# Kernel tuning notes

Hardware: AMD Instinct MI355X
Metric: run time of the kernel (lower is better)

The kernel has to match this reference:

```python
import jax, jax.numpy as jnp
import numpy as np

B, N, CQ, CH, H = 4, 1024, 512, 512, 8
D = CH // H  # head_dim = 64


def setup_inputs() -> dict:
    key = jax.random.key(0)
    ks = jax.random.split(key, 8)
    s = jnp.float32(0.02)  # realistic (non-degenerate) init scale instead of the module's zeros
    return {
        "q_x": jax.random.normal(ks[0], (B, N, CQ), jnp.float32),
        "attn_bias": jax.random.normal(ks[1], (B, H, N, N), jnp.float32),
        "Wq": jax.random.normal(ks[2], (CH, CQ), jnp.float32) * s,
        "bq": jnp.zeros((CH,), jnp.float32),
        "Wk": jax.random.normal(ks[3], (CH, CQ), jnp.float32) * s,  # LinearNoBias
        "Wv": jax.random.normal(ks[4], (CH, CQ), jnp.float32) * s,  # LinearNoBias
        "Wo": jax.random.normal(ks[5], (CQ, CH), jnp.float32) * s,
        "bo": jnp.zeros((CQ,), jnp.float32),
        "Wg": jax.random.normal(ks[6], (CQ, CQ), jnp.float32) * s,
        "bg": jnp.zeros((CQ,), jnp.float32),
        "gating_bias": jnp.ones((CQ,), jnp.float32),
    }


def reference(q_x, attn_bias, Wq, bq, Wk, Wv, Wo, bo, Wg, bg, gating_bias):
    Bq, Nq, _ = q_x.shape
    scale = jnp.asarray(D, q_x.dtype) ** -0.5
    # QKV projections; self-attention path (q_x is kv_x, ndim==3) applies scale to q
    q = (q_x @ Wq.T + bq).reshape(Bq, Nq, H, D).transpose(0, 2, 1, 3) * scale  # [B,H,N,D]
    k = (q_x @ Wk.T).reshape(Bq, Nq, H, D).transpose(0, 2, 1, 3)               # [B,H,N,D]
    v = (q_x @ Wv.T).reshape(Bq, Nq, H, D).transpose(0, 2, 1, 3)               # [B,H,N,D]
    # bias-augmented attention
    logits = jnp.einsum("bhqd,bhkd->bhqk", q, k) + attn_bias                    # [B,H,N,N]
    a = jax.nn.softmax(logits, axis=-1)
    o = jnp.einsum("bhqk,bhkd->bhqd", a, v)                                     # [B,H,N,D]
    o = o.transpose(0, 2, 1, 3).reshape(Bq, Nq, CH)                             # flatten heads
    out = o @ Wo.T + bo                                                         # to_out: c_hidden -> c_q
    # sigmoid gating with learned gating_bias (init ones)
    gate = jax.nn.sigmoid(q_x @ Wg.T + bg + gating_bias)
    return out * gate
```

## Files before the change

### kernel.cpp

```cpp
#include <hip/hip_runtime.h>
#include <math.h>


typedef __bf16 bf16x8 __attribute__((ext_vector_type(8)));
typedef float f32x4 __attribute__((ext_vector_type(4)));

__device__ __forceinline__ unsigned short f2bf(float f) {
    union { float f; unsigned u; } v; v.f = f;
    unsigned r = v.u + 0x7fff + ((v.u >> 16) & 1);
    return (unsigned short)(r >> 16);
}

__device__ __forceinline__ bf16x8 ldb8(const unsigned short* p) {
    union { float4 f; bf16x8 b; } u;
    u.f = *(const float4*)p;
    return u.b;
}

__device__ __forceinline__ void ld16(unsigned short* l, const unsigned short* g) {
    __builtin_amdgcn_global_load_lds(
        (const __attribute__((address_space(1))) unsigned*)g,
        (__attribute__((address_space(3))) unsigned*)l, 16, 0, 0);
}

__global__ __launch_bounds__(256) void convert_kernel(
    const float* __restrict__ X, const float* __restrict__ Wq,
    const float* __restrict__ Wk, const float* __restrict__ Wg,
    const float* __restrict__ Wv, const float* __restrict__ Wo,
    unsigned short* __restrict__ Xb, unsigned short* __restrict__ Wcat)
{
    int i4 = (blockIdx.x * 256 + threadIdx.x) * 4;
    const float* src;
    unsigned short* dst;
    int off;
    if (i4 < 2097152) {
        src = X; dst = Xb; off = i4;
    } else {
        int g = i4 - 2097152;
        int sect = g >> 18;
        src = (sect == 0) ? Wq : (sect == 1) ? Wk : (sect == 2) ? Wg
            : (sect == 3) ? Wv : Wo;
        dst = Wcat + (sect << 18);
        off = g & 262143;
    }
    float4 v = *(const float4*)&src[off];
    ushort4 u;
    u.x = f2bf(v.x); u.y = f2bf(v.y); u.z = f2bf(v.z); u.w = f2bf(v.w);
    *(ushort4*)&dst[off] = u;
}

__device__ __forceinline__ void gemm_core(
    const unsigned short* __restrict__ Ag,
    const unsigned short* __restrict__ Bg,
    unsigned short* __restrict__ Ab, unsigned short* __restrict__ Bb,
    f32x4 acc[4][4])
{
    const int tid = threadIdx.x;
    const int lane = tid & 63;
    const int quad = lane >> 4, lx = lane & 15;
    const int wid = tid >> 6;
    const int mw0 = (wid >> 1) * 64, nw0 = (wid & 1) * 64;
    const int r0 = tid >> 2, c0 = (tid & 3) * 8;
    const int r1 = (tid + 256) >> 2, c1 = (tid & 3) * 8;
    unsigned short* lA0 = Ab + ((tid & ~63) << 3);
    unsigned short* lA1 = Ab + (((tid & ~63) + 256) << 3);
    unsigned short* lB0 = Bb + ((tid & ~63) << 3);
    unsigned short* lB1 = Bb + (((tid & ~63) + 256) << 3);

    for (int k0 = 0; k0 < 512; k0 += 32) {
        ld16(lA0, &Ag[(size_t)r0 * 512 + k0 + c0]);
        ld16(lA1, &Ag[(size_t)r1 * 512 + k0 + c1]);
        ld16(lB0, &Bg[(size_t)r0 * 512 + k0 + c0]);
        ld16(lB1, &Bg[(size_t)r1 * 512 + k0 + c1]);
        __syncthreads();
        bf16x8 af[4], bfr[4];
#pragma unroll
        for (int mi = 0; mi < 4; ++mi)
            af[mi] = ldb8(&Ab[(mw0 + mi * 16 + lx) * 32 + quad * 8]);
#pragma unroll
        for (int ni = 0; ni < 4; ++ni)
            bfr[ni] = ldb8(&Bb[(nw0 + ni * 16 + lx) * 32 + quad * 8]);
#pragma unroll
        for (int mi = 0; mi < 4; ++mi)
#pragma unroll
            for (int ni = 0; ni < 4; ++ni)
                acc[mi][ni] = __builtin_amdgcn_mfma_f32_16x16x32_bf16(
                    af[mi], bfr[ni], acc[mi][ni], 0, 0, 0);
        __syncthreads();
    }
}

__global__ __launch_bounds__(256) void proj_gemm(
    const unsigned short* __restrict__ Xb, const unsigned short* __restrict__ Wcat,
    const float* __restrict__ bq, const float* __restrict__ bg,
    const float* __restrict__ gbias,
    unsigned short* __restrict__ qb, unsigned short* __restrict__ kb,
    unsigned short* __restrict__ vtb, float* __restrict__ gateb)
{
    __shared__ __align__(16) unsigned short Ab[128 * 32];
    __shared__ __align__(16) unsigned short Bb[128 * 32];
    const int row0 = blockIdx.x * 128;
    const int colv0 = blockIdx.y * 128;
    f32x4 acc[4][4];
#pragma unroll
    for (int i = 0; i < 4; ++i)
#pragma unroll
        for (int j = 0; j < 4; ++j) acc[i][j] = (f32x4){0.f, 0.f, 0.f, 0.f};

    gemm_core(Xb + (size_t)row0 * 512, Wcat + (size_t)colv0 * 512, Ab, Bb, acc);

    const int tid = threadIdx.x;
    const int lane = tid & 63;
    const int quad = lane >> 4, lx = lane & 15;
    const int wid = tid >> 6;
    const int mw0 = (wid >> 1) * 64, nw0 = (wid & 1) * 64;
    const int wsel = colv0 >> 9;
    const int ncb = colv0 & 511;

    if (wsel == 0) {
#pragma unroll
        for (int mi = 0; mi < 4; ++mi) {
#pragma unroll
            for (int ni = 0; ni < 4; ++ni) {
                int ch = ncb + nw0 + ni * 16 + lx;
                int h = ch >> 6, d = ch & 63;
                float bias = bq[ch];
#pragma unroll
                for (int r = 0; r < 4; ++r) {
                    int m = row0 + mw0 + mi * 16 + quad * 4 + r;
                    int b = m >> 10, nn = m & 1023;
                    qb[(size_t)(b * 8 + h) * 65536 + (size_t)nn * 64 + d] =
                        f2bf((acc[mi][ni][r] + bias) * 0.125f);
                }
            }
        }
    } else if (wsel == 1) {
#pragma unroll
        for (int mi = 0; mi < 4; ++mi) {
#pragma unroll
            for (int ni = 0; ni < 4; ++ni) {
                int ch = ncb + nw0 + ni * 16 + lx;
                int h = ch >> 6, d = ch & 63;
#pragma unroll
                for (int r = 0; r < 4; ++r) {
                    int m = row0 + mw0 + mi * 16 + quad * 4 + r;
                    int b = m >> 10, nn = m & 1023;
                    kb[(size_t)(b * 8 + h) * 65536 + (size_t)nn * 64 + d] =
                        f2bf(acc[mi][ni][r]);
                }
            }
        }
    } else if (wsel == 2) {
#pragma unroll
        for (int mi = 0; mi < 4; ++mi) {
#pragma unroll
            for (int ni = 0; ni < 4; ++ni) {
                int ch = ncb + nw0 + ni * 16 + lx;
                float bias = bg[ch] + gbias[ch];
#pragma unroll
                for (int r = 0; r < 4; ++r) {
                    int m = row0 + mw0 + mi * 16 + quad * 4 + r;
                    float z = acc[mi][ni][r] + bias;
                    gateb[(size_t)m * 512 + ch] = 1.f / (1.f + __expf(-z));
                }
            }
        }
    } else {
#pragma unroll
        for (int mi = 0; mi < 4; ++mi) {
            int tok0 = row0 + mw0 + mi * 16 + quad * 4;
            int b = tok0 >> 10, nn0 = tok0 & 1023;
#pragma unroll
            for (int ni = 0; ni < 4; ++ni) {
                int ch = ncb + nw0 + ni * 16 + lx;
                int h = ch >> 6, d = ch & 63;
                ushort4 u;
                u.x = f2bf(acc[mi][ni][0]);
                u.y = f2bf(acc[mi][ni][1]);
                u.z = f2bf(acc[mi][ni][2]);
                u.w = f2bf(acc[mi][ni][3]);
                *(ushort4*)&vtb[(size_t)(b * 8 + h) * 65536 + (size_t)d * 1024 + nn0] = u;
            }
        }
    }
}

#define LSTR 72

__global__ __launch_bounds__(256) void attn_kernel(
    const unsigned short* __restrict__ qb, const unsigned short* __restrict__ kb,
    const unsigned short* __restrict__ vtb, const float* __restrict__ bias,
    unsigned short* __restrict__ obb)
{
    __shared__ unsigned short Qs[64 * LSTR];
    __shared__ unsigned short Ks[64 * LSTR];
    __shared__ unsigned short Vt[64 * LSTR];
    __shared__ unsigned short Ps[64 * LSTR];

    const int tid = threadIdx.x;
    const int bh = blockIdx.y;
    const int qr0 = blockIdx.x * 64;
    const int wv = tid >> 6, lane = tid & 63;
    const int quad = lane >> 4, lx = lane & 15;
    const int qw0 = wv * 16;

    const unsigned short* qp = qb + (size_t)bh * 65536;
    const unsigned short* kp = kb + (size_t)bh * 65536;
    const unsigned short* vp = vtb + (size_t)bh * 65536;
    const float* bp = bias + (size_t)bh * 1048576;

    const int sr0 = tid >> 3, sc0 = (tid & 7) * 8;
    const int sr1 = (tid + 256) >> 3, sc1 = (tid & 7) * 8;

    *(float4*)&Qs[sr0 * LSTR + sc0] = *(const float4*)&qp[(size_t)(qr0 + sr0) * 64 + sc0];
    *(float4*)&Qs[sr1 * LSTR + sc1] = *(const float4*)&qp[(size_t)(qr0 + sr1) * 64 + sc1];

    float4 kr0 = *(const float4*)&kp[(size_t)sr0 * 64 + sc0];
    float4 kr1 = *(const float4*)&kp[(size_t)sr1 * 64 + sc1];
    float4 vr0 = *(const float4*)&vp[(size_t)sr0 * 1024 + sc0];
    float4 vr1 = *(const float4*)&vp[(size_t)sr1 * 1024 + sc1];

    const float* bbase = bp + (size_t)(qr0 + qw0 + quad * 4) * 1024 + lx;
    float bv[4][4];
#pragma unroll
    for (int r = 0; r < 4; ++r)
#pragma unroll
        for (int c = 0; c < 4; ++c)
            bv[r][c] = bbase[(size_t)r * 1024 + c * 16];

    __syncthreads();

    bf16x8 aq0 = ldb8(&Qs[(qw0 + lx) * LSTR + quad * 8]);
    bf16x8 aq1 = ldb8(&Qs[(qw0 + lx) * LSTR + 32 + quad * 8]);

    float l_i[4] = {0.f, 0.f, 0.f, 0.f};
    f32x4 oacc[4];
#pragma unroll
    for (int c = 0; c < 4; ++c) oacc[c] = (f32x4){0.f, 0.f, 0.f, 0.f};

#pragma unroll 1
    for (int kt = 0; kt < 16; ++kt) {
        __syncthreads();
        *(float4*)&Ks[sr0 * LSTR + sc0] = kr0;
        *(float4*)&Ks[sr1 * LSTR + sc1] = kr1;
        *(float4*)&Vt[sr0 * LSTR + sc0] = vr0;
        *(float4*)&Vt[sr1 * LSTR + sc1] = vr1;
        __syncthreads();

        const int ktn = (kt + 1) & 15;
        kr0 = *(const float4*)&kp[(size_t)(ktn * 64 + sr0) * 64 + sc0];
        kr1 = *(const float4*)&kp[(size_t)(ktn * 64 + sr1) * 64 + sc1];
        vr0 = *(const float4*)&vp[(size_t)sr0 * 1024 + ktn * 64 + sc0];
        vr1 = *(const float4*)&vp[(size_t)sr1 * 1024 + ktn * 64 + sc1];
        float bvn[4][4];
#pragma unroll
        for (int r = 0; r < 4; ++r)
#pragma unroll
            for (int c = 0; c < 4; ++c)
                bvn[r][c] = bbase[(size_t)r * 1024 + ktn * 64 + c * 16];

        f32x4 sacc[4];
#pragma unroll
        for (int c = 0; c < 4; ++c) {
            bf16x8 bk0 = ldb8(&Ks[(c * 16 + lx) * LSTR + quad * 8]);
            bf16x8 bk1 = ldb8(&Ks[(c * 16 + lx) * LSTR + 32 + quad * 8]);
            f32x4 z = {0.f, 0.f, 0.f, 0.f};
            z = __builtin_amdgcn_mfma_f32_16x16x32_bf16(aq0, bk0, z, 0, 0, 0);
            z = __builtin_amdgcn_mfma_f32_16x16x32_bf16(aq1, bk1, z, 0, 0, 0);
            sacc[c] = z;
        }

#pragma unroll
        for (int r = 0; r < 4; ++r) {
            float p0 = __expf(sacc[0][r] + bv[r][0]);
            float p1 = __expf(sacc[1][r] + bv[r][1]);
            float p2 = __expf(sacc[2][r] + bv[r][2]);
            float p3 = __expf(sacc[3][r] + bv[r][3]);
            l_i[r] += p0 + p1 + p2 + p3;
            int prow = (qw0 + quad * 4 + r) * LSTR;
            Ps[prow + 0 * 16 + lx] = f2bf(p0);
            Ps[prow + 1 * 16 + lx] = f2bf(p1);
            Ps[prow + 2 * 16 + lx] = f2bf(p2);
            Ps[prow + 3 * 16 + lx] = f2bf(p3);
        }

        bf16x8 ap0 = ldb8(&Ps[(qw0 + lx) * LSTR + quad * 8]);
        bf16x8 ap1 = ldb8(&Ps[(qw0 + lx) * LSTR + 32 + quad * 8]);
#pragma unroll
        for (int c = 0; c < 4; ++c) {
            bf16x8 bv0 = ldb8(&Vt[(c * 16 + lx) * LSTR + quad * 8]);
            bf16x8 bv1 = ldb8(&Vt[(c * 16 + lx) * LSTR + 32 + quad * 8]);
            oacc[c] = __builtin_amdgcn_mfma_f32_16x16x32_bf16(ap0, bv0, oacc[c], 0, 0, 0);
            oacc[c] = __builtin_amdgcn_mfma_f32_16x16x32_bf16(ap1, bv1, oacc[c], 0, 0, 0);
        }

#pragma unroll
        for (int r = 0; r < 4; ++r)
#pragma unroll
            for (int c = 0; c < 4; ++c)
                bv[r][c] = bvn[r][c];
    }

    const int b = bh >> 3, h = bh & 7;
#pragma unroll
    for (int r = 0; r < 4; ++r) {
        float lt = l_i[r];
        lt += __shfl_xor(lt, 1);
        lt += __shfl_xor(lt, 2);
        lt += __shfl_xor(lt, 4);
        lt += __shfl_xor(lt, 8);
        float inv = 1.f / lt;
        int row = qr0 + qw0 + quad * 4 + r;
        unsigned short* op = obb + (size_t)(b * 1024 + row) * 512 + h * 64 + lx;
#pragma unroll
        for (int c = 0; c < 4; ++c)
            op[c * 16] = f2bf(oacc[c][r] * inv);
    }
}

__global__ __launch_bounds__(256) void out_gemm(
    const unsigned short* __restrict__ obb, const unsigned short* __restrict__ WoB,
    const float* __restrict__ bo, const float* __restrict__ gateb,
    float* __restrict__ out)
{
    __shared__ __align__(16) unsigned short Ab[128 * 32];
    __shared__ __align__(16) unsigned short Bb[128 * 32];
    const int row0 = blockIdx.x * 128;
    const int n0 = blockIdx.y * 128;
    f32x4 acc[4][4];
#pragma unroll
    for (int i = 0; i < 4; ++i)
#pragma unroll
        for (int j = 0; j < 4; ++j) acc[i][j] = (f32x4){0.f, 0.f, 0.f, 0.f};

    gemm_core(obb + (size_t)row0 * 512, WoB + (size_t)n0 * 512, Ab, Bb, acc);

    const int tid = threadIdx.x;
    const int lane = tid & 63;
    const int quad = lane >> 4, lx = lane & 15;
    const int wid = tid >> 6;
    const int mw0 = (wid >> 1) * 64, nw0 = (wid & 1) * 64;

#pragma unroll
    for (int mi = 0; mi < 4; ++mi) {
#pragma unroll
        for (int ni = 0; ni < 4; ++ni) {
            int n = n0 + nw0 + ni * 16 + lx;
            float bias = bo[n];
#pragma unroll
            for (int r = 0; r < 4; ++r) {
                int m = row0 + mw0 + mi * 16 + quad * 4 + r;
                out[(size_t)m * 512 + n] =
                    (acc[mi][ni][r] + bias) * gateb[(size_t)m * 512 + n];
            }
        }
    }
}

extern "C" void kernel_launch(void* const* d_in, const int* in_sizes, int n_in,
                              void* d_out, int out_size, void* d_ws, size_t ws_size,
                              hipStream_t stream) {
    (void)in_sizes; (void)n_in; (void)out_size; (void)ws_size;
    const float* q_x   = (const float*)d_in[0];
    const float* bias  = (const float*)d_in[1];
    const float* Wq    = (const float*)d_in[2];
    const float* bq    = (const float*)d_in[3];
    const float* Wk    = (const float*)d_in[4];
    const float* Wv    = (const float*)d_in[5];
    const float* Wo    = (const float*)d_in[6];
    const float* bo    = (const float*)d_in[7];
    const float* Wg    = (const float*)d_in[8];
    const float* bg    = (const float*)d_in[9];
    const float* gbias = (const float*)d_in[10];
    float* out = (float*)d_out;

    char* ws = (char*)d_ws;
    unsigned short* qb   = (unsigned short*)ws;
    unsigned short* kb   = (unsigned short*)(ws + (4u << 20));
    unsigned short* vtb  = (unsigned short*)(ws + (8u << 20));
    float* gateb         = (float*)(ws + (12u << 20));
    unsigned short* obb  = (unsigned short*)(ws + (20u << 20));
    unsigned short* Xb   = (unsigned short*)(ws + (24u << 20));
    unsigned short* Wcat = (unsigned short*)(ws + (28u << 20));

    convert_kernel<<<3328, 256, 0, stream>>>(q_x, Wq, Wk, Wg, Wv, Wo, Xb, Wcat);
    proj_gemm<<<dim3(32, 16), dim3(256), 0, stream>>>(
        Xb, Wcat, bq, bg, gbias, qb, kb, vtb, gateb);
    attn_kernel<<<dim3(16, 32), dim3(256), 0, stream>>>(qb, kb, vtb, bias, obb);
    out_gemm<<<dim3(32, 4), dim3(256), 0, stream>>>(
        obb, Wcat + (size_t)2048 * 512, bo, gateb, out);
}
```

Measured before the change: 268.4 us.

## Register-prefetch GEMM tiles into padded LDS, shrink out_gemm tile, merge attn buffers

The GEMM core stops using direct global-to-LDS loads. It now prefetches the next K-slice into registers while the MFMAs run on the current one, and stores tiles with a padded stride to cut bank conflicts. out_gemm switches to 64-row tiles, doubling its grid so more CUs get work. The attention kernel reuses the Q buffer for P to cut shared memory, which could raise occupancy. The register prefetch adds register pressure and costs VGPR-to-LDS store instructions.

```diff
diff --git a/kernel.cpp b/kernel.cpp
--- a/kernel.cpp
+++ b/kernel.cpp
@@ -15,12 +15,6 @@
     union { float4 f; bf16x8 b; } u;
     u.f = *(const float4*)p;
     return u.b;
-}
-
-__device__ __forceinline__ void ld16(unsigned short* l, const unsigned short* g) {
-    __builtin_amdgcn_global_load_lds(
-        (const __attribute__((address_space(1))) unsigned*)g,
-        (__attribute__((address_space(3))) unsigned*)l, 16, 0, 0);
 }
 
 __global__ __launch_bounds__(256) void convert_kernel(
@@ -49,6 +43,8 @@
     *(ushort4*)&dst[off] = u;
 }
 
+#define GSTR 40
+
 __device__ __forceinline__ void gemm_core(
     const unsigned short* __restrict__ Ag,
     const unsigned short* __restrict__ Bg,
@@ -60,26 +56,36 @@
     const int quad = lane >> 4, lx = lane & 15;
     const int wid = tid >> 6;
     const int mw0 = (wid >> 1) * 64, nw0 = (wid & 1) * 64;
-    const int r0 = tid >> 2, c0 = (tid & 3) * 8;
-    const int r1 = (tid + 256) >> 2, c1 = (tid & 3) * 8;
-    unsigned short* lA0 = Ab + ((tid & ~63) << 3);
-    unsigned short* lA1 = Ab + (((tid & ~63) + 256) << 3);
-    unsigned short* lB0 = Bb + ((tid & ~63) << 3);
-    unsigned short* lB1 = Bb + (((tid & ~63) + 256) << 3);
-
+    const int rA = tid >> 2, cA = (tid & 3) * 8;
+    const int l0 = rA * GSTR + cA;
+    const int l1 = (rA + 64) * GSTR + cA;
+
+    float4 a0 = *(const float4*)&Ag[(size_t)rA * 512 + cA];
+    float4 a1 = *(const float4*)&Ag[(size_t)(rA + 64) * 512 + cA];
+    float4 b0 = *(const float4*)&Bg[(size_t)rA * 512 + cA];
+    float4 b1 = *(const float4*)&Bg[(size_t)(rA + 64) * 512 + cA];
+
+#pragma unroll 1
     for (int k0 = 0; k0 < 512; k0 += 32) {
-        ld16(lA0, &Ag[(size_t)r0 * 512 + k0 + c0]);
-        ld16(lA1, &Ag[(size_t)r1 * 512 + k0 + c1]);
-        ld16(lB0, &Bg[(size_t)r0 * 512 + k0 + c0]);
-        ld16(lB1, &Bg[(size_t)r1 * 512 + k0 + c1]);
-        __syncthreads();
+        *(float4*)&Ab[l0] = a0;
+        *(float4*)&Ab[l1] = a1;
+        *(float4*)&Bb[l0] = b0;
+        *(float4*)&Bb[l1] = b1;
+        __syncthreads();
+        if (k0 < 480) {
+            int kn = k0 + 32;
+            a0 = *(const float4*)&Ag[(size_t)rA * 512 + kn + cA];
+            a1 = *(const float4*)&Ag[(size_t)(rA + 64) * 512 + kn + cA];
+            b0 = *(const float4*)&Bg[(size_t)rA * 512 + kn + cA];
+            b1 = *(const float4*)&Bg[(size_t)(rA + 64) * 512 + kn + cA];
+        }
         bf16x8 af[4], bfr[4];
 #pragma unroll
         for (int mi = 0; mi < 4; ++mi)
-            af[mi] = ldb8(&Ab[(mw0 + mi * 16 + lx) * 32 + quad * 8]);
+            af[mi] = ldb8(&Ab[(mw0 + mi * 16 + lx) * GSTR + quad * 8]);
 #pragma unroll
         for (int ni = 0; ni < 4; ++ni)
-            bfr[ni] = ldb8(&Bb[(nw0 + ni * 16 + lx) * 32 + quad * 8]);
+            bfr[ni] = ldb8(&Bb[(nw0 + ni * 16 + lx) * GSTR + quad * 8]);
 #pragma unroll
         for (int mi = 0; mi < 4; ++mi)
 #pragma unroll
@@ -97,8 +103,8 @@
     unsigned short* __restrict__ qb, unsigned short* __restrict__ kb,
     unsigned short* __restrict__ vtb, float* __restrict__ gateb)
 {
-    __shared__ __align__(16) unsigned short Ab[128 * 32];
-    __shared__ __align__(16) unsigned short Bb[128 * 32];
+    __shared__ __align__(16) unsigned short Ab[128 * GSTR];
+    __shared__ __align__(16) unsigned short Bb[128 * GSTR];
     const int row0 = blockIdx.x * 128;
     const int colv0 = blockIdx.y * 128;
     f32x4 acc[4][4];
@@ -192,10 +198,9 @@
     const unsigned short* __restrict__ vtb, const float* __restrict__ bias,
     unsigned short* __restrict__ obb)
 {
-    __shared__ unsigned short Qs[64 * LSTR];
+    __shared__ unsigned short QPs[64 * LSTR];
     __shared__ unsigned short Ks[64 * LSTR];
     __shared__ unsigned short Vt[64 * LSTR];
-    __shared__ unsigned short Ps[64 * LSTR];
 
     const int tid = threadIdx.x;
     const int bh = blockIdx.y;
@@ -212,8 +217,8 @@
     const int sr0 = tid >> 3, sc0 = (tid & 7) * 8;
     const int sr1 = (tid + 256) >> 3, sc1 = (tid & 7) * 8;
 
-    *(float4*)&Qs[sr0 * LSTR + sc0] = *(const float4*)&qp[(size_t)(qr0 + sr0) * 64 + sc0];
-    *(float4*)&Qs[sr1 * LSTR + sc1] = *(const float4*)&qp[(size_t)(qr0 + sr1) * 64 + sc1];
+    *(float4*)&QPs[sr0 * LSTR + sc0] = *(const float4*)&qp[(size_t)(qr0 + sr0) * 64 + sc0];
+    *(float4*)&QPs[sr1 * LSTR + sc1] = *(const float4*)&qp[(size_t)(qr0 + sr1) * 64 + sc1];
 
     float4 kr0 = *(const float4*)&kp[(size_t)sr0 * 64 + sc0];
     float4 kr1 = *(const float4*)&kp[(size_t)sr1 * 64 + sc1];
@@ -230,8 +235,8 @@
 
     __syncthreads();
 
-    bf16x8 aq0 = ldb8(&Qs[(qw0 + lx) * LSTR + quad * 8]);
-    bf16x8 aq1 = ldb8(&Qs[(qw0 + lx) * LSTR + 32 + quad * 8]);
+    bf16x8 aq0 = ldb8(&QPs[(qw0 + lx) * LSTR + quad * 8]);
+    bf16x8 aq1 = ldb8(&QPs[(qw0 + lx) * LSTR + 32 + quad * 8]);
 
     float l_i[4] = {0.f, 0.f, 0.f, 0.f};
     f32x4 oacc[4];
@@ -278,14 +283,14 @@
             float p3 = __expf(sacc[3][r] + bv[r][3]);
             l_i[r] += p0 + p1 + p2 + p3;
             int prow = (qw0 + quad * 4 + r) * LSTR;
-            Ps[prow + 0 * 16 + lx] = f2bf(p0);
-            Ps[prow + 1 * 16 + lx] = f2bf(p1);
-            Ps[prow + 2 * 16 + lx] = f2bf(p2);
-            Ps[prow + 3 * 16 + lx] = f2bf(p3);
-        }
-
-        bf16x8 ap0 = ldb8(&Ps[(qw0 + lx) * LSTR + quad * 8]);
-        bf16x8 ap1 = ldb8(&Ps[(qw0 + lx) * LSTR + 32 + quad * 8]);
+            QPs[prow + 0 * 16 + lx] = f2bf(p0);
+            QPs[prow + 1 * 16 + lx] = f2bf(p1);
+            QPs[prow + 2 * 16 + lx] = f2bf(p2);
+            QPs[prow + 3 * 16 + lx] = f2bf(p3);
+        }
+
+        bf16x8 ap0 = ldb8(&QPs[(qw0 + lx) * LSTR + quad * 8]);
+        bf16x8 ap1 = ldb8(&QPs[(qw0 + lx) * LSTR + 32 + quad * 8]);
 #pragma unroll
         for (int c = 0; c < 4; ++c) {
             bf16x8 bv0 = ldb8(&Vt[(c * 16 + lx) * LSTR + quad * 8]);
@@ -319,30 +324,67 @@
 }
 
 __global__ __launch_bounds__(256) void out_gemm(
-    const unsigned short* __restrict__ obb, const unsigned short* __restrict__ WoB,
+    const unsigned short* __restrict__ A, const unsigned short* __restrict__ WoB,
     const float* __restrict__ bo, const float* __restrict__ gateb,
     float* __restrict__ out)
 {
-    __shared__ __align__(16) unsigned short Ab[128 * 32];
-    __shared__ __align__(16) unsigned short Bb[128 * 32];
-    const int row0 = blockIdx.x * 128;
+    __shared__ __align__(16) unsigned short Ab[64 * GSTR];
+    __shared__ __align__(16) unsigned short Bb[128 * GSTR];
+    const int tid = threadIdx.x;
+    const int row0 = blockIdx.x * 64;
     const int n0 = blockIdx.y * 128;
-    f32x4 acc[4][4];
-#pragma unroll
-    for (int i = 0; i < 4; ++i)
-#pragma unroll
-        for (int j = 0; j < 4; ++j) acc[i][j] = (f32x4){0.f, 0.f, 0.f, 0.f};
-
-    gemm_core(obb + (size_t)row0 * 512, WoB + (size_t)n0 * 512, Ab, Bb, acc);
-
-    const int tid = threadIdx.x;
+    const unsigned short* Ag = A + (size_t)row0 * 512;
+    const unsigned short* Bg = WoB + (size_t)n0 * 512;
+
     const int lane = tid & 63;
     const int quad = lane >> 4, lx = lane & 15;
     const int wid = tid >> 6;
-    const int mw0 = (wid >> 1) * 64, nw0 = (wid & 1) * 64;
-
-#pragma unroll
-    for (int mi = 0; mi < 4; ++mi) {
+    const int mw0 = (wid & 1) * 32, nw0 = (wid >> 1) * 64;
+    const int rA = tid >> 2, cA = (tid & 3) * 8;
+    const int lA = rA * GSTR + cA;
+    const int lB0 = lA;
+    const int lB1 = (rA + 64) * GSTR + cA;
+
+    f32x4 acc[2][4];
+#pragma unroll
+    for (int i = 0; i < 2; ++i)
+#pragma unroll
+        for (int j = 0; j < 4; ++j) acc[i][j] = (f32x4){0.f, 0.f, 0.f, 0.f};
+
+    float4 a0 = *(const float4*)&Ag[(size_t)rA * 512 + cA];
+    float4 b0 = *(const float4*)&Bg[(size_t)rA * 512 + cA];
+    float4 b1 = *(const float4*)&Bg[(size_t)(rA + 64) * 512 + cA];
+
+#pragma unroll 1
+    for (int k0 = 0; k0 < 512; k0 += 32) {
+        *(float4*)&Ab[lA] = a0;
+        *(float4*)&Bb[lB0] = b0;
+        *(float4*)&Bb[lB1] = b1;
+        __syncthreads();
+        if (k0 < 480) {
+            int kn = k0 + 32;
+            a0 = *(const float4*)&Ag[(size_t)rA * 512 + kn + cA];
+            b0 = *(const float4*)&Bg[(size_t)rA * 512 + kn + cA];
+            b1 = *(const float4*)&Bg[(size_t)(rA + 64) * 512 + kn + cA];
+        }
+        bf16x8 af[2], bfr[4];
+#pragma unroll
+        for (int mi = 0; mi < 2; ++mi)
+            af[mi] = ldb8(&Ab[(mw0 + mi * 16 + lx) * GSTR + quad * 8]);
+#pragma unroll
+        for (int ni = 0; ni < 4; ++ni)
+            bfr[ni] = ldb8(&Bb[(nw0 + ni * 16 + lx) * GSTR + quad * 8]);
+#pragma unroll
+        for (int mi = 0; mi < 2; ++mi)
+#pragma unroll
+            for (int ni = 0; ni < 4; ++ni)
+                acc[mi][ni] = __builtin_amdgcn_mfma_f32_16x16x32_bf16(
+                    af[mi], bfr[ni], acc[mi][ni], 0, 0, 0);
+        __syncthreads();
+    }
+
+#pragma unroll
+    for (int mi = 0; mi < 2; ++mi) {
 #pragma unroll
         for (int ni = 0; ni < 4; ++ni) {
             int n = n0 + nw0 + ni * 16 + lx;
@@ -387,6 +429,6 @@
     proj_gemm<<<dim3(32, 16), dim3(256), 0, stream>>>(
         Xb, Wcat, bq, bg, gbias, qb, kb, vtb, gateb);
     attn_kernel<<<dim3(16, 32), dim3(256), 0, stream>>>(qb, kb, vtb, bias, obb);
-    out_gemm<<<dim3(32, 4), dim3(256), 0, stream>>>(
+    out_gemm<<<dim3(64, 4), dim3(256), 0, stream>>>(
         obb, Wcat + (size_t)2048 * 512, bo, gateb, out);
 }
```

New measurement: 266.2 us. About the same (-0.8%).
